# Optimization experiments

Hardware: AMD Instinct MI355X
Metric: run time of the kernel (lower is better)

## Reference

```python
import jax, jax.numpy as jnp
import numpy as np

D_MODEL = 1024
N_HEAD = 16
D_QKV = 64
INIT_RANGE = 0.02
BOUND = float(np.sqrt(3.0) * INIT_RANGE)
SCALE = 1.0 / D_QKV ** 0.5


def setup_inputs() -> dict:
    key = jax.random.key(0)
    kx, k1, k2, k3, k4 = jax.random.split(key, 5)
    B, T = 4, 2048
    x = jax.random.normal(kx, (B, T, D_MODEL), dtype=jnp.float32)
    half_f = D_MODEL // 2
    half_a = D_QKV // 2
    u = lambda k, shp: jax.random.uniform(k, shp, dtype=jnp.float32, minval=-BOUND, maxval=BOUND)
    w_qkv_c = u(k1, (N_HEAD, half_f, 3, half_a))
    w_qkv_p = u(k2, (N_HEAD, half_f, 3, half_a))
    w_o_c = u(k3, (N_HEAD, half_a, half_f))
    w_o_p = u(k4, (N_HEAD, half_a, half_f))
    return {"x": x, "w_qkv_c": w_qkv_c, "w_qkv_p": w_qkv_p, "w_o_c": w_o_c, "w_o_p": w_o_p}


def reference(x, w_qkv_c, w_qkv_p, w_o_c, w_o_p):
    x_c, x_p = jnp.split(x, 2, axis=-1)  # [B,T,d_model//2] each
    # partitioned QKV projections: [B,H,T,3,a/2]
    qkv_c = jnp.einsum('btf,hfca->bhtca', x_c, w_qkv_c)
    qkv_p = jnp.einsum('btf,hfca->bhtca', x_p, w_qkv_p)
    q_c, k_c, v_c = qkv_c[:, :, :, 0], qkv_c[:, :, :, 1], qkv_c[:, :, :, 2]
    q_p, k_p, v_p = qkv_p[:, :, :, 0], qkv_p[:, :, :, 1], qkv_p[:, :, :, 2]
    q = jnp.concatenate([q_c, q_p], axis=-1) * SCALE  # [B,H,T,d_qkv]
    k = jnp.concatenate([k_c, k_p], axis=-1)
    v = jnp.concatenate([v_c, v_p], axis=-1)
    dots = jnp.einsum('bhqa,bhka->bhqk', q, k)  # [B,H,T,T]
    probs = jax.nn.softmax(dots, axis=-1)
    o = jnp.einsum('bhqk,bhka->bhqa', probs, v)  # [B,H,T,d_qkv]
    o_c, o_p = jnp.split(o, 2, axis=-1)
    out_c = jnp.einsum('bhta,haf->btf', o_c, w_o_c)
    out_p = jnp.einsum('bhta,haf->btf', o_p, w_o_p)
    return (out_c, out_p)
```

## Files before the change

### kernel.cpp

```cpp
#include <hip/hip_runtime.h>


typedef __attribute__((ext_vector_type(8))) short bf16x8;
typedef __attribute__((ext_vector_type(4))) float f32x4;
typedef unsigned short u16;

#define QSCALE 0.18033688011112042f

__device__ __forceinline__ u16 f2bf(float f){
  unsigned u = __builtin_bit_cast(unsigned, f);
  u += 0x7FFFu + ((u >> 16) & 1u);
  return (u16)(u >> 16);
}

__device__ __forceinline__ unsigned cvtpk(float lo, float hi){
  unsigned r;
  asm("v_cvt_pk_bf16_f32 %0, %1, %2" : "=v"(r) : "v"(lo), "v"(hi));
  return r;
}

__device__ __forceinline__ void gload16(const void* g, void* l){
  __builtin_amdgcn_global_load_lds(
    (const __attribute__((address_space(1))) unsigned*)g,
    (__attribute__((address_space(3))) unsigned*)l, 16, 0, 0);
}

__global__ __launch_bounds__(256) void k_cvt_x(const float4* __restrict__ x, u16* __restrict__ xA){
  unsigned i = blockIdx.x*256 + threadIdx.x;
  float4 v = x[i];
  unsigned j = i*4;
  unsigned row = j >> 10, col = j & 1023u;
  unsigned tile = row >> 4, li = row & 15u;
  unsigned part = col >> 9, ks = (col >> 5) & 15u, lg = (col >> 3) & 3u, e = col & 7u;
  uint2 pk;
  pk.x = (unsigned)f2bf(v.x) | ((unsigned)f2bf(v.y) << 16);
  pk.y = (unsigned)f2bf(v.z) | ((unsigned)f2bf(v.w) << 16);
  *(uint2*)(xA + (size_t)(((tile*2 + part)*16 + ks)*512) + li*32 + lg*8 + e) = pk;
}

__global__ __launch_bounds__(256) void k_repack_qkv(const float* __restrict__ wc, const float* __restrict__ wp,
                                                    u16* __restrict__ wt){
  unsigned i = blockIdx.x*256 + threadIdx.x;
  unsigned ph = i / 49152u;
  unsigned r  = i - ph*49152u;
  unsigned ks = r / 3072u;
  unsigned r2 = r - ks*3072u;
  unsigned n  = r2 >> 9;
  unsigned r3 = r2 & 511u;
  unsigned lg = r3 >> 7, li = (r3 >> 3) & 15u, e = r3 & 7u;
  unsigned h = ph & 15u;
  unsigned f = ks*32u + lg*8u + e;
  const float* src = (ph < 16) ? wc : wp;
  wt[i] = f2bf(src[h*49152u + f*96u + (n>>1)*32u + (n&1u)*16u + li]);
}

__global__ __launch_bounds__(256) void k_repack_wo(const float* __restrict__ wc, const float* __restrict__ wp,
                                                   u16* __restrict__ wt){
  unsigned i = blockIdx.x*256 + threadIdx.x;
  unsigned e = i & 7u;
  unsigned lane = (i >> 3) & 63u;
  unsigned n  = (i >> 9) & 7u;
  unsigned ks = (i >> 12) & 15u;
  unsigned ft = (i >> 16) & 3u;
  unsigned part = i >> 18;
  unsigned f = ft*128u + n*16u + (lane & 15u);
  unsigned a = (lane >> 4)*8u + e;
  const float* src = part ? wp : wc;
  wt[i] = f2bf(src[ks*16384u + a*512u + f]);
}

__global__ __launch_bounds__(256) void k_qkv(const u16* __restrict__ xA, const u16* __restrict__ wt,
                                             u16* __restrict__ Q, u16* __restrict__ K, u16* __restrict__ VT){
  const int lane = threadIdx.x & 63, wv = threadIdx.x >> 6;
  const int lg = lane >> 4, li = lane & 15;
  const int blk = blockIdx.x;
  const int xcd = blk & 7, idx = blk >> 3;
  const int tt  = (idx >> 5)*8 + xcd;
  const int ph  = idx & 31;
  const int row0 = tt*256 + wv*64;
  const int part = ph >> 4, h = ph & 15;

  f32x4 acc[4][6] = {};
  const u16* wbase = wt + (size_t)ph*49152;
  const unsigned aoff = (unsigned)(li*32 + lg*8);
  #pragma unroll 2
  for (int ks = 0; ks < 16; ++ks){
    bf16x8 a[4], b[6];
    #pragma unroll
    for (int m=0;m<4;++m)
      a[m] = *(const bf16x8*)(xA + (size_t)(((tt*16 + wv*4 + m)*2 + part)*16 + ks)*512 + aoff);
    #pragma unroll
    for (int n=0;n<6;++n)
      b[n] = *(const bf16x8*)(wbase + ks*3072 + n*512 + lane*8);
    #pragma unroll
    for (int m=0;m<4;++m)
      #pragma unroll
      for (int n=0;n<6;++n)
        acc[m][n] = __builtin_amdgcn_mfma_f32_16x16x32_bf16(a[m], b[n], acc[m][n], 0, 0, 0);
  }

  const int b_ = row0 >> 11;
  const int bh = b_*16 + h;
  const int tl0 = (row0 & 2047) + lg*4;
  #pragma unroll
  for (int m=0;m<4;++m){
    #pragma unroll
    for (int n=0;n<6;++n){
      const int c = n >> 1;
      const int af = part*32 + (n & 1)*16 + li;
      if (c == 2){
        uint2 pk;
        pk.x = (unsigned)f2bf(acc[m][n][0]) | ((unsigned)f2bf(acc[m][n][1]) << 16);
        pk.y = (unsigned)f2bf(acc[m][n][2]) | ((unsigned)f2bf(acc[m][n][3]) << 16);
        *(uint2*)(VT + (size_t)(bh*64 + af)*2048 + tl0 + m*16) = pk;
      } else {
        u16* dst = (c == 0) ? Q : K;
        const float sc = (c == 0) ? QSCALE : 1.0f;
        #pragma unroll
        for (int r=0;r<4;++r){
          int tl = tl0 + m*16 + r;
          dst[((size_t)bh*2048 + tl)*64 + af] = f2bf(acc[m][n][r] * sc);
        }
      }
    }
  }
}

#define NKT 64
#define PLD 40
__global__ __launch_bounds__(256, 4) void k_attn(const u16* __restrict__ Q, const u16* __restrict__ K,
                                                 const u16* __restrict__ VT, u16* __restrict__ OA){
  __shared__ __align__(16) char smem[36864];
  const int lane = threadIdx.x & 63, w = threadIdx.x >> 6;
  const int lg = lane >> 4, li = lane & 15;
  const int swz = (blockIdx.x & 7)*128 + (blockIdx.x >> 3);
  const int bh = swz >> 4, qt = swz & 15;
  const int q0 = qt*128 + w*32;

  const char* Kg = (const char*)(K  + (size_t)bh*131072);
  const char* Vg = (const char*)(VT + (size_t)bh*131072);
  const u16*  Qb = Q + (size_t)bh*131072;
  u16* pw = (u16*)(smem + 16384) + w*2560;

  const unsigned ksrc = (unsigned)((w*8 + (lane>>3))*128 + (((lane&7) ^ (lane>>3)) << 4));
  const unsigned vsrc0 = (unsigned)((w*16 + (lane>>2))*4096 + (((lane&3) ^ ((lane>>2)&3)) << 4));
  const unsigned ldst = (unsigned)(w*1024);

  const unsigned kc0 = (unsigned)(((     lg) ^ (li&7)) << 4);
  const unsigned kc1 = (unsigned)(((4 +  lg) ^ (li&7)) << 4);
  const unsigned vc  = (unsigned)(((lg) ^ (li&3)) << 4);

  bf16x8 aq[2][2];
  #pragma unroll
  for (int m=0;m<2;++m)
    #pragma unroll
    for (int kd=0;kd<2;++kd)
      aq[m][kd] = *(const bf16x8*)(Qb + (size_t)(q0 + m*16 + li)*64 + kd*32 + lg*8);

  const short one_bf = (short)0x3F80;
  bf16x8 ones = {one_bf,one_bf,one_bf,one_bf,one_bf,one_bf,one_bf,one_bf};

  f32x4 o[2][4] = {};
  f32x4 ls[2] = {};

  auto QKEXP = [&](const char* sK, u16* pW){
    #pragma unroll
    for (int n=0;n<2;++n){
      bf16x8 bk0 = *(const bf16x8*)(sK + (n*16 + li)*128 + kc0);
      bf16x8 bk1 = *(const bf16x8*)(sK + (n*16 + li)*128 + kc1);
      #pragma unroll
      for (int m=0;m<2;++m){
        f32x4 s = {0.f,0.f,0.f,0.f};
        s = __builtin_amdgcn_mfma_f32_16x16x32_bf16(bk0, aq[m][0], s, 0, 0, 0);
        s = __builtin_amdgcn_mfma_f32_16x16x32_bf16(bk1, aq[m][1], s, 0, 0, 0);
        uint2 pk;
        pk.x = cvtpk(__builtin_exp2f(s[0]), __builtin_exp2f(s[1]));
        pk.y = cvtpk(__builtin_exp2f(s[2]), __builtin_exp2f(s[3]));
        *(uint2*)(pW + (size_t)(m*16 + li)*PLD + n*16 + lg*4) = pk;
      }
    }
  };
  auto PV = [&](const char* sV, const u16* pR){
    bf16x8 pa0 = *(const bf16x8*)(pR + (size_t)(     li)*PLD + lg*8);
    bf16x8 pa1 = *(const bf16x8*)(pR + (size_t)(16 + li)*PLD + lg*8);
    __builtin_amdgcn_s_setprio(1);
    #pragma unroll
    for (int nd=0;nd<4;++nd){
      bf16x8 bv = *(const bf16x8*)(sV + (nd*16 + li)*64 + vc);
      o[0][nd] = __builtin_amdgcn_mfma_f32_16x16x32_bf16(pa0, bv, o[0][nd], 0, 0, 0);
      o[1][nd] = __builtin_amdgcn_mfma_f32_16x16x32_bf16(pa1, bv, o[1][nd], 0, 0, 0);
    }
    ls[0] = __builtin_amdgcn_mfma_f32_16x16x32_bf16(pa0, ones, ls[0], 0, 0, 0);
    ls[1] = __builtin_amdgcn_mfma_f32_16x16x32_bf16(pa1, ones, ls[1], 0, 0, 0);
    __builtin_amdgcn_s_setprio(0);
  };

  gload16(Kg + ksrc,          smem + ldst);
  gload16(Vg + vsrc0,         smem + 8192 + ldst);
  gload16(Kg + 4096u + ksrc,  smem + 4096 + ldst);
  asm volatile("s_waitcnt vmcnt(0)" ::: "memory");
  __builtin_amdgcn_s_barrier();
  QKEXP(smem, pw);
  __builtin_amdgcn_s_barrier();

  for (int kt = 0; kt < NKT-1; ++kt){
    const int pr = kt & 1, pn = pr ^ 1;
    gload16(Vg + (kt+1)*64u + vsrc0, smem + 8192 + pn*4096 + ldst);
    if (kt + 2 < NKT)
      gload16(Kg + (kt+2)*4096u + ksrc, smem + pr*4096 + ldst);
    QKEXP(smem + pn*4096, pw + pn*1280);
    PV(smem + 8192 + pr*4096, pw + pr*1280);
    asm volatile("s_waitcnt vmcnt(0)" ::: "memory");
    __builtin_amdgcn_s_barrier();
  }
  PV(smem + 8192 + ((NKT-1)&1)*4096, pw + ((NKT-1)&1)*1280);

  const int b_ = bh >> 4, h = bh & 15;
  #pragma unroll
  for (int m=0;m<2;++m){
    const int tile = (b_*2048 + q0 + m*16) >> 4;
    #pragma unroll
    for (int r=0;r<4;++r){
      float linv = 1.0f / ls[m][r];
      #pragma unroll
      for (int nd=0;nd<4;++nd){
        OA[(size_t)(((tile*16 + h)*2 + (nd>>1))*512)
           + (lg*4 + r)*32 + ((nd&1)*2 + (li>>3))*8 + (li&7)] = f2bf(o[m][nd][r] * linv);
      }
    }
  }
}

__global__ __launch_bounds__(256) void k_proj(const u16* __restrict__ OA, const u16* __restrict__ wot,
                                              float* __restrict__ out){
  const int lane = threadIdx.x & 63, wv = threadIdx.x >> 6;
  const int lg = lane >> 4, li = lane & 15;
  const int blk = blockIdx.x;
  const int xcd = blk & 7, idx = blk >> 3;
  const int rowTile = (idx >> 3)*8 + xcd;
  const int colTile = idx & 7;
  const int row0 = rowTile*128 + wv*32;
  const int part = colTile >> 2;
  const int ft   = colTile & 3;
  const int f0   = ft*128;

  f32x4 acc[2][8] = {};
  const u16* wbase = wot + (size_t)part*262144 + (size_t)ft*65536;
  const unsigned aoff = (unsigned)(li*32 + lg*8);
  #pragma unroll 4
  for (int ks = 0; ks < 16; ++ks){
    bf16x8 a[2];
    #pragma unroll
    for (int m=0;m<2;++m)
      a[m] = *(const bf16x8*)(OA + (size_t)((((rowTile*8 + wv*2 + m)*16 + ks)*2 + part)*512) + aoff);
    #pragma unroll
    for (int n=0;n<8;++n){
      bf16x8 b = *(const bf16x8*)(wbase + ks*4096 + n*512 + lane*8);
      #pragma unroll
      for (int m=0;m<2;++m)
        acc[m][n] = __builtin_amdgcn_mfma_f32_16x16x32_bf16(a[m], b, acc[m][n], 0, 0, 0);
    }
  }
  float* obp = out + (size_t)part*(8192u*512u);
  #pragma unroll
  for (int m=0;m<2;++m)
    #pragma unroll
    for (int n=0;n<8;++n)
      #pragma unroll
      for (int r=0;r<4;++r)
        obp[(size_t)(row0 + m*16 + lg*4 + r)*512 + f0 + n*16 + li] = acc[m][n][r];
}

extern "C" void kernel_launch(void* const* d_in, const int* in_sizes, int n_in,
                              void* d_out, int out_size, void* d_ws, size_t ws_size,
                              hipStream_t stream){
  const float* x   = (const float*)d_in[0];
  const float* wqc = (const float*)d_in[1];
  const float* wqp = (const float*)d_in[2];
  const float* woc = (const float*)d_in[3];
  const float* wop = (const float*)d_in[4];

  char* ws = (char*)d_ws;
  u16* xA  = (u16*)(ws);
  u16* Q   = (u16*)(ws + 16777216);
  u16* K   = (u16*)(ws + 2*16777216);
  u16* VT  = (u16*)(ws + 3*16777216);
  u16* wqt = (u16*)(ws + 4*16777216);
  u16* wot = (u16*)(ws + 4*16777216 + 3145728);
  u16* OA  = xA;
  float* out = (float*)d_out;

  k_cvt_x     <<<8192, 256, 0, stream>>>((const float4*)x, xA);
  k_repack_qkv<<<6144, 256, 0, stream>>>(wqc, wqp, wqt);
  k_repack_wo <<<2048, 256, 0, stream>>>(woc, wop, wot);
  k_qkv       <<<1024, 256, 0, stream>>>(xA, wqt, Q, K, VT);
  k_attn      <<<1024, 256, 0, stream>>>(Q, K, VT, OA);
  k_proj      <<<512,  256, 0, stream>>>(OA, wot, out);
}
```

Measured before the change: 178.9 us.

## Merge prep kernels into one launch and pre-tile V for contiguous loads

The three conversion and repack kernels become a single launch that branches on block index, removing two kernel launches and the gaps between them. The QKV kernel now writes V^T already split into 32-key tiles with the LDS XOR swizzle applied, so the attention kernel fetches each V tile as one contiguous 4KB chunk instead of strided 64-byte rows. This trades scattered global loads in the hot attention loop for a more complex scatter pattern in the QKV epilogue.

```diff
diff --git a/kernel.cpp b/kernel.cpp
--- a/kernel.cpp
+++ b/kernel.cpp
@@ -25,48 +25,49 @@
     (__attribute__((address_space(3))) unsigned*)l, 16, 0, 0);
 }
 
-__global__ __launch_bounds__(256) void k_cvt_x(const float4* __restrict__ x, u16* __restrict__ xA){
-  unsigned i = blockIdx.x*256 + threadIdx.x;
-  float4 v = x[i];
-  unsigned j = i*4;
-  unsigned row = j >> 10, col = j & 1023u;
-  unsigned tile = row >> 4, li = row & 15u;
-  unsigned part = col >> 9, ks = (col >> 5) & 15u, lg = (col >> 3) & 3u, e = col & 7u;
-  uint2 pk;
-  pk.x = (unsigned)f2bf(v.x) | ((unsigned)f2bf(v.y) << 16);
-  pk.y = (unsigned)f2bf(v.z) | ((unsigned)f2bf(v.w) << 16);
-  *(uint2*)(xA + (size_t)(((tile*2 + part)*16 + ks)*512) + li*32 + lg*8 + e) = pk;
-}
-
-__global__ __launch_bounds__(256) void k_repack_qkv(const float* __restrict__ wc, const float* __restrict__ wp,
-                                                    u16* __restrict__ wt){
-  unsigned i = blockIdx.x*256 + threadIdx.x;
-  unsigned ph = i / 49152u;
-  unsigned r  = i - ph*49152u;
-  unsigned ks = r / 3072u;
-  unsigned r2 = r - ks*3072u;
-  unsigned n  = r2 >> 9;
-  unsigned r3 = r2 & 511u;
-  unsigned lg = r3 >> 7, li = (r3 >> 3) & 15u, e = r3 & 7u;
-  unsigned h = ph & 15u;
-  unsigned f = ks*32u + lg*8u + e;
-  const float* src = (ph < 16) ? wc : wp;
-  wt[i] = f2bf(src[h*49152u + f*96u + (n>>1)*32u + (n&1u)*16u + li]);
-}
-
-__global__ __launch_bounds__(256) void k_repack_wo(const float* __restrict__ wc, const float* __restrict__ wp,
-                                                   u16* __restrict__ wt){
-  unsigned i = blockIdx.x*256 + threadIdx.x;
-  unsigned e = i & 7u;
-  unsigned lane = (i >> 3) & 63u;
-  unsigned n  = (i >> 9) & 7u;
-  unsigned ks = (i >> 12) & 15u;
-  unsigned ft = (i >> 16) & 3u;
-  unsigned part = i >> 18;
-  unsigned f = ft*128u + n*16u + (lane & 15u);
-  unsigned a = (lane >> 4)*8u + e;
-  const float* src = part ? wp : wc;
-  wt[i] = f2bf(src[ks*16384u + a*512u + f]);
+__global__ __launch_bounds__(256) void k_prep(const float4* __restrict__ x, u16* __restrict__ xA,
+                                              const float* __restrict__ wqc, const float* __restrict__ wqp,
+                                              u16* __restrict__ wqt,
+                                              const float* __restrict__ woc, const float* __restrict__ wop,
+                                              u16* __restrict__ wot){
+  const unsigned blk = blockIdx.x;
+  if (blk < 8192u){
+    unsigned i = blk*256 + threadIdx.x;
+    float4 v = x[i];
+    unsigned j = i*4;
+    unsigned row = j >> 10, col = j & 1023u;
+    unsigned tile = row >> 4, li = row & 15u;
+    unsigned part = col >> 9, ks = (col >> 5) & 15u, lg = (col >> 3) & 3u, e = col & 7u;
+    uint2 pk;
+    pk.x = (unsigned)f2bf(v.x) | ((unsigned)f2bf(v.y) << 16);
+    pk.y = (unsigned)f2bf(v.z) | ((unsigned)f2bf(v.w) << 16);
+    *(uint2*)(xA + (size_t)(((tile*2 + part)*16 + ks)*512) + li*32 + lg*8 + e) = pk;
+  } else if (blk < 14336u){
+    unsigned i = (blk - 8192u)*256 + threadIdx.x;
+    unsigned ph = i / 49152u;
+    unsigned r  = i - ph*49152u;
+    unsigned ks = r / 3072u;
+    unsigned r2 = r - ks*3072u;
+    unsigned n  = r2 >> 9;
+    unsigned r3 = r2 & 511u;
+    unsigned lg = r3 >> 7, li = (r3 >> 3) & 15u, e = r3 & 7u;
+    unsigned h = ph & 15u;
+    unsigned f = ks*32u + lg*8u + e;
+    const float* src = (ph < 16) ? wqc : wqp;
+    wqt[i] = f2bf(src[h*49152u + f*96u + (n>>1)*32u + (n&1u)*16u + li]);
+  } else {
+    unsigned i = (blk - 14336u)*256 + threadIdx.x;
+    unsigned e = i & 7u;
+    unsigned lane = (i >> 3) & 63u;
+    unsigned n  = (i >> 9) & 7u;
+    unsigned ks = (i >> 12) & 15u;
+    unsigned ft = (i >> 16) & 3u;
+    unsigned part = i >> 18;
+    unsigned f = ft*128u + n*16u + (lane & 15u);
+    unsigned a = (lane >> 4)*8u + e;
+    const float* src = part ? wop : woc;
+    wot[i] = f2bf(src[ks*16384u + a*512u + f]);
+  }
 }
 
 __global__ __launch_bounds__(256) void k_qkv(const u16* __restrict__ xA, const u16* __restrict__ wt,
@@ -112,7 +113,11 @@
         uint2 pk;
         pk.x = (unsigned)f2bf(acc[m][n][0]) | ((unsigned)f2bf(acc[m][n][1]) << 16);
         pk.y = (unsigned)f2bf(acc[m][n][2]) | ((unsigned)f2bf(acc[m][n][3]) << 16);
-        *(uint2*)(VT + (size_t)(bh*64 + af)*2048 + tl0 + m*16) = pk;
+        const int c2 = (m&1)*2 + (lg>>1);
+        char* dst = (char*)VT + (size_t)bh*262144
+                  + (size_t)(((row0 & 2047) >> 5) + (m>>1))*4096
+                  + af*64 + ((c2 ^ (af&3))<<4) + (lg&1)*8;
+        *(uint2*)dst = pk;
       } else {
         u16* dst = (c == 0) ? Q : K;
         const float sc = (c == 0) ? QSCALE : 1.0f;
@@ -137,13 +142,13 @@
   const int bh = swz >> 4, qt = swz & 15;
   const int q0 = qt*128 + w*32;
 
-  const char* Kg = (const char*)(K  + (size_t)bh*131072);
-  const char* Vg = (const char*)(VT + (size_t)bh*131072);
+  const char* Kg = (const char*)(K + (size_t)bh*131072);
+  const char* Vg = (const char*)VT + (size_t)bh*262144;
   const u16*  Qb = Q + (size_t)bh*131072;
   u16* pw = (u16*)(smem + 16384) + w*2560;
 
   const unsigned ksrc = (unsigned)((w*8 + (lane>>3))*128 + (((lane&7) ^ (lane>>3)) << 4));
-  const unsigned vsrc0 = (unsigned)((w*16 + (lane>>2))*4096 + (((lane&3) ^ ((lane>>2)&3)) << 4));
+  const unsigned vsrc = (unsigned)(w*1024 + lane*16);
   const unsigned ldst = (unsigned)(w*1024);
 
   const unsigned kc0 = (unsigned)(((     lg) ^ (li&7)) << 4);
@@ -196,7 +201,7 @@
   };
 
   gload16(Kg + ksrc,          smem + ldst);
-  gload16(Vg + vsrc0,         smem + 8192 + ldst);
+  gload16(Vg + vsrc,          smem + 8192 + ldst);
   gload16(Kg + 4096u + ksrc,  smem + 4096 + ldst);
   asm volatile("s_waitcnt vmcnt(0)" ::: "memory");
   __builtin_amdgcn_s_barrier();
@@ -205,7 +210,7 @@
 
   for (int kt = 0; kt < NKT-1; ++kt){
     const int pr = kt & 1, pn = pr ^ 1;
-    gload16(Vg + (kt+1)*64u + vsrc0, smem + 8192 + pn*4096 + ldst);
+    gload16(Vg + (kt+1)*4096u + vsrc, smem + 8192 + pn*4096 + ldst);
     if (kt + 2 < NKT)
       gload16(Kg + (kt+2)*4096u + ksrc, smem + pr*4096 + ldst);
     QKEXP(smem + pn*4096, pw + pn*1280);
@@ -290,10 +295,8 @@
   u16* OA  = xA;
   float* out = (float*)d_out;
 
-  k_cvt_x     <<<8192, 256, 0, stream>>>((const float4*)x, xA);
-  k_repack_qkv<<<6144, 256, 0, stream>>>(wqc, wqp, wqt);
-  k_repack_wo <<<2048, 256, 0, stream>>>(woc, wop, wot);
-  k_qkv       <<<1024, 256, 0, stream>>>(xA, wqt, Q, K, VT);
-  k_attn      <<<1024, 256, 0, stream>>>(Q, K, VT, OA);
-  k_proj      <<<512,  256, 0, stream>>>(OA, wot, out);
-}
+  k_prep <<<16384, 256, 0, stream>>>((const float4*)x, xA, wqc, wqp, wqt, woc, wop, wot);
+  k_qkv  <<<1024,  256, 0, stream>>>(xA, wqt, Q, K, VT);
+  k_attn <<<1024,  256, 0, stream>>>(Q, K, VT, OA);
+  k_proj <<<512,   256, 0, stream>>>(OA, wot, out);
+}
```

After: 174.2 us. -2.6%, faster.
